# Optimization experiments

Hardware: AMD Instinct MI355X
Metric: run time of the kernel (lower is better)

Reference implementation:

```python
import jax, jax.numpy as jnp
import numpy as np

N, C, H = 256, 128, 4
D = C // H


def setup_inputs() -> dict:
    key = jax.random.key(0)
    ks = jax.random.split(key, 7)
    pair_rep = jax.random.normal(ks[0], (N, N, C), dtype=jnp.float32)
    distance_matrix = jax.random.normal(ks[1], (N, N), dtype=jnp.float32)
    Wqkv = jax.random.normal(ks[2], (C, 3 * C), dtype=jnp.float32) * (1.0 / np.sqrt(C))
    bqkv = jax.random.normal(ks[3], (3 * C,), dtype=jnp.float32) * 0.02
    Wout = jax.random.normal(ks[4], (C, C), dtype=jnp.float32) * (1.0 / np.sqrt(C))
    bout = jax.random.normal(ks[5], (C,), dtype=jnp.float32) * 0.02
    dscale = jnp.ones((1,), dtype=jnp.float32)
    mask = jax.random.randint(ks[6], (N, N), 0, 2).astype(jnp.bool_)
    return {"pair_rep": pair_rep, "distance_matrix": distance_matrix, "Wqkv": Wqkv,
            "bqkv": bqkv, "Wout": Wout, "bout": bout, "dscale": dscale, "mask": mask}


def reference(pair_rep, distance_matrix, Wqkv, bqkv, Wout, bout, dscale, mask):
    n = pair_rep.shape[0]
    qkv = pair_rep @ Wqkv + bqkv                      # [n,n,3c]
    q, k, v = jnp.split(qkv, 3, axis=-1)
    q = q.reshape(n, n, H, D)
    k = k.reshape(n, n, H, D)
    v = v.reshape(n, n, H, D)
    # scores[h,i,j,k] = q[i,j,h,:] . k[i,k,h,:] / sqrt(D)
    scores = jnp.einsum('ijhd,ikhd->hijk', q, k) / np.sqrt(D)
    bias = (dscale[0] * distance_matrix)[None, None, :, :]   # [1,1,n,n]
    scores = scores + bias
    scores = jnp.where(mask[None, None, :, :], -jnp.inf, scores)
    attn = jax.nn.softmax(scores, axis=-1)            # [H,n,n,n]
    out = jnp.einsum('hijk,ikhd->ijhd', attn, v).reshape(n, n, C)
    return out @ Wout + bout
```

## Files before the change

### kernel.cpp

```cpp
#include <hip/hip_runtime.h>
#include <hip/hip_bf16.h>
#include <math.h>

#define NN 256
#define CC 128
#define HH 4
#define DD 32

typedef uint4 u128;
typedef __bf16 bf16x8 __attribute__((ext_vector_type(8)));
typedef float f32x4 __attribute__((ext_vector_type(4)));

#define LOG2E 1.4426950408889634f
#define QSC (0.17677669529663687f * LOG2E)

__global__ __launch_bounds__(256) void prep_kernel(
    const float* __restrict__ dm, const int* __restrict__ mask,
    const float* __restrict__ dscale,
    const float* __restrict__ Wqkv, const float* __restrict__ Wout,
    float* __restrict__ bias2,
    __hip_bfloat16* __restrict__ Wt_qkv, __hip_bfloat16* __restrict__ Wt_out)
{
    const int b = blockIdx.x, t = threadIdx.x;
    if (b < 256) {
        const int j = b, k = t;
        int idx = j * 256 + k;
        float v = mask[idx] ? -INFINITY : dscale[0] * dm[idx] * LOG2E;
        int c = k >> 5, bb = (k >> 4) & 1, quad = (k >> 2) & 3, r = k & 3;
        int dst = ((((c * 2 + bb) * 16 + (j >> 4)) * 64) + quad * 16 + (j & 15)) * 4 + r;
        bias2[dst] = v;
    } else if (b < 448) {
        int idx = (b - 256) * 256 + t;
        int n = idx >> 7, k = idx & 127;
        Wt_qkv[idx] = __float2bfloat16(Wqkv[(size_t)k * 384 + n]);
    } else {
        int idx = (b - 448) * 256 + t;
        int n = idx >> 7, k = idx & 127;
        Wt_out[idx] = __float2bfloat16(Wout[(size_t)k * CC + n]);
    }
}

__global__ __launch_bounds__(512, 2) void qkv_mfma_kernel(
    const float* __restrict__ A,
    const __hip_bfloat16* __restrict__ Bt,
    const float* __restrict__ bias,
    __hip_bfloat16* __restrict__ out)
{
    __shared__ __align__(16) __hip_bfloat16 As[128][136];
    __shared__ __align__(16) __hip_bfloat16 Bs[96][136];
    const int t = threadIdx.x;
    const int m0 = blockIdx.x * 128;

    float4 va[8];
    #pragma unroll
    for (int it = 0; it < 8; ++it) {
        int idx = it * 512 + t;
        int r = idx >> 5, c4 = (idx & 31) * 4;
        va[it] = *(const float4*)(A + (size_t)(m0 + r) * CC + c4);
    }
    #pragma unroll
    for (int it = 0; it < 8; ++it) {
        int idx = it * 512 + t;
        int r = idx >> 5, c4 = (idx & 31) * 4;
        __hip_bfloat162 a01 = __float22bfloat162_rn(float2{va[it].x, va[it].y});
        __hip_bfloat162 a23 = __float22bfloat162_rn(float2{va[it].z, va[it].w});
        uint2 pk;
        pk.x = *(unsigned int*)&a01;
        pk.y = *(unsigned int*)&a23;
        *(uint2*)&As[r][c4] = pk;
    }
    #pragma unroll
    for (int it = 0; it < 3; ++it) {
        int idx = it * 512 + t;
        int n = idx >> 4, c8 = (idx & 15) * 8;
        *(u128*)&Bs[n][c8] = *(const u128*)(Bt + (size_t)n * CC + c8);
    }
    __syncthreads();

    const int w = t >> 6, lane = t & 63;
    const int n16 = lane & 15, quad = lane >> 4;
    const int mw = (w & 3) * 32, nw = (w >> 2) * 48;

    bf16x8 pf[2][4];
    #pragma unroll
    for (int mt = 0; mt < 2; ++mt)
        #pragma unroll
        for (int ks = 0; ks < 4; ++ks)
            pf[mt][ks] = *(const bf16x8*)&As[mw + mt * 16 + n16][ks * 32 + quad * 8];

    for (int nc = 0; nc < 4; ++nc) {
        const int n0 = nc * 96;

        f32x4 acc[2][3];
        #pragma unroll
        for (int mt = 0; mt < 2; ++mt)
            #pragma unroll
            for (int nt = 0; nt < 3; ++nt) acc[mt][nt] = (f32x4){0.f, 0.f, 0.f, 0.f};

        #pragma unroll
        for (int nt = 0; nt < 3; ++nt) {
            bf16x8 wf[4];
            #pragma unroll
            for (int ks = 0; ks < 4; ++ks)
                wf[ks] = *(const bf16x8*)&Bs[nw + nt * 16 + n16][ks * 32 + quad * 8];
            #pragma unroll
            for (int ks = 0; ks < 4; ++ks)
                #pragma unroll
                for (int mt = 0; mt < 2; ++mt)
                    acc[mt][nt] = __builtin_amdgcn_mfma_f32_16x16x32_bf16(wf[ks], pf[mt][ks], acc[mt][nt], 0, 0, 0);
        }
        __syncthreads();

        u128 breg[3];
        if (nc < 3) {
            #pragma unroll
            for (int it = 0; it < 3; ++it) {
                int idx = it * 512 + t;
                int n = idx >> 4, c8 = (idx & 15) * 8;
                breg[it] = *(const u128*)(Bt + (size_t)(n0 + 96 + n) * CC + c8);
            }
        }

        #pragma unroll
        for (int nt = 0; nt < 3; ++nt) {
            int nbase = n0 + nw + nt * 16 + quad * 4;
            float4 b4 = *(const float4*)(bias + nbase);
            float sc = (nbase < CC) ? QSC : 1.0f;
            #pragma unroll
            for (int mt = 0; mt < 2; ++mt) {
                int m = m0 + mw + mt * 16 + n16;
                __hip_bfloat162 h01 = __float22bfloat162_rn(float2{(acc[mt][nt][0] + b4.x) * sc, (acc[mt][nt][1] + b4.y) * sc});
                __hip_bfloat162 h23 = __float22bfloat162_rn(float2{(acc[mt][nt][2] + b4.z) * sc, (acc[mt][nt][3] + b4.w) * sc});
                uint2 pk;
                pk.x = *(unsigned int*)&h01;
                pk.y = *(unsigned int*)&h23;
                *(uint2*)&out[(size_t)m * 384 + nbase] = pk;
            }
        }

        if (nc < 3) {
            #pragma unroll
            for (int it = 0; it < 3; ++it) {
                int idx = it * 512 + t;
                int n = idx >> 4, c8 = (idx & 15) * 8;
                *(u128*)&Bs[n][c8] = breg[it];
            }
            __syncthreads();
        }
    }
}

__global__ __launch_bounds__(512, 8) void attn_mfma_kernel(
    const __hip_bfloat16* __restrict__ qkv,
    const float* __restrict__ bias2,
    __hip_bfloat16* __restrict__ attn_out)
{
    __shared__ __align__(16) __hip_bfloat16 Ks[NN][40];
    __shared__ __align__(16) __hip_bfloat16 VTs[DD][264];

    const int bi = blockIdx.x;
    const int i = bi >> 2, h = bi & 3;
    const int t = threadIdx.x;

    {
        const int r = t >> 1, half = t & 1;
        const __hip_bfloat16* base = qkv + (size_t)(i * NN + r) * 384 + h * DD;
        const u128* ksrc = (const u128*)(base + CC) + half * 2;
        u128* kdst = (u128*)&Ks[r][0] + half * 2;
        kdst[0] = ksrc[0];
        kdst[1] = ksrc[1];
        const u128* vsrc = (const u128*)(base + 2 * CC) + half * 2;
        u128 vr[2];
        vr[0] = vsrc[0];
        vr[1] = vsrc[1];
        const __hip_bfloat16* vh = (const __hip_bfloat16*)vr;
        const int pr = (r & ~0x1F) | ((r & 0xC) << 1) | ((r & 0x10) >> 2) | (r & 0x3);
        #pragma unroll
        for (int dd = 0; dd < 16; ++dd) VTs[half * 16 + dd][pr] = vh[dd];
    }
    __syncthreads();

    const int w = t >> 6, lane = t & 63;
    const int n16 = lane & 15, quad = lane >> 4;

    #pragma unroll
    for (int jt = 0; jt < 2; ++jt) {
        const int j0 = w * 32 + jt * 16;
        const int j = j0 + n16;
        const int jblk = w * 2 + jt;

        bf16x8 qa = *(const bf16x8*)(qkv + (size_t)(i * NN + j) * 384 + h * DD + quad * 8);
        const float4* bb = (const float4*)bias2;

        f32x4 sm = {0.f, 0.f, 0.f, 0.f};
        f32x4 o0 = {0.f, 0.f, 0.f, 0.f}, o1 = {0.f, 0.f, 0.f, 0.f};

        #pragma unroll 2
        for (int c = 0; c < 8; ++c) {
            float4 b0 = bb[((c * 2 + 0) * 16 + jblk) * 64 + lane];
            float4 b1 = bb[((c * 2 + 1) * 16 + jblk) * 64 + lane];
            bf16x8 kb0 = *(const bf16x8*)&Ks[c * 32 + n16][quad * 8];
            bf16x8 kb1 = *(const bf16x8*)&Ks[c * 32 + 16 + n16][quad * 8];
            f32x4 s0 = __builtin_amdgcn_mfma_f32_16x16x32_bf16(
                kb0, qa, (f32x4){b0.x, b0.y, b0.z, b0.w}, 0, 0, 0);
            f32x4 s1 = __builtin_amdgcn_mfma_f32_16x16x32_bf16(
                kb1, qa, (f32x4){b1.x, b1.y, b1.z, b1.w}, 0, 0, 0);

            float p0 = __builtin_amdgcn_exp2f(s0[0]);
            float p1 = __builtin_amdgcn_exp2f(s0[1]);
            float p2 = __builtin_amdgcn_exp2f(s0[2]);
            float p3 = __builtin_amdgcn_exp2f(s0[3]);
            float p4 = __builtin_amdgcn_exp2f(s1[0]);
            float p5 = __builtin_amdgcn_exp2f(s1[1]);
            float p6 = __builtin_amdgcn_exp2f(s1[2]);
            float p7 = __builtin_amdgcn_exp2f(s1[3]);
            sm[0] += p0 + p4;
            sm[1] += p1 + p5;
            sm[2] += p2 + p6;
            sm[3] += p3 + p7;

            __hip_bfloat162 q01 = __float22bfloat162_rn(float2{p0, p1});
            __hip_bfloat162 q23 = __float22bfloat162_rn(float2{p2, p3});
            __hip_bfloat162 q45 = __float22bfloat162_rn(float2{p4, p5});
            __hip_bfloat162 q67 = __float22bfloat162_rn(float2{p6, p7});
            u128 pk;
            pk.x = *(unsigned int*)&q01;
            pk.y = *(unsigned int*)&q23;
            pk.z = *(unsigned int*)&q45;
            pk.w = *(unsigned int*)&q67;
            bf16x8 pa = *(bf16x8*)&pk;

            bf16x8 vb0 = *(const bf16x8*)&VTs[n16][c * 32 + quad * 8];
            bf16x8 vb1 = *(const bf16x8*)&VTs[16 + n16][c * 32 + quad * 8];
            o0 = __builtin_amdgcn_mfma_f32_16x16x32_bf16(vb0, pa, o0, 0, 0, 0);
            o1 = __builtin_amdgcn_mfma_f32_16x16x32_bf16(vb1, pa, o1, 0, 0, 0);
        }

        float sum = (sm[0] + sm[1]) + (sm[2] + sm[3]);
        sum += __shfl_xor(sum, 16);
        sum += __shfl_xor(sum, 32);
        float inv = 1.0f / sum;

        __hip_bfloat16* obase = attn_out + (size_t)(i * NN + j) * CC + h * DD + quad * 4;
        {
            __hip_bfloat162 h01 = __float22bfloat162_rn(float2{o0[0] * inv, o0[1] * inv});
            __hip_bfloat162 h23 = __float22bfloat162_rn(float2{o0[2] * inv, o0[3] * inv});
            uint2 pk;
            pk.x = *(unsigned int*)&h01;
            pk.y = *(unsigned int*)&h23;
            *(uint2*)(obase) = pk;
        }
        {
            __hip_bfloat162 h01 = __float22bfloat162_rn(float2{o1[0] * inv, o1[1] * inv});
            __hip_bfloat162 h23 = __float22bfloat162_rn(float2{o1[2] * inv, o1[3] * inv});
            uint2 pk;
            pk.x = *(unsigned int*)&h01;
            pk.y = *(unsigned int*)&h23;
            *(uint2*)(obase + 16) = pk;
        }
    }
}

__global__ __launch_bounds__(512, 4) void out_mfma_kernel(
    const __hip_bfloat16* __restrict__ A,
    const __hip_bfloat16* __restrict__ Bt,
    const float* __restrict__ bias,
    float* __restrict__ out)
{
    __shared__ __align__(16) __hip_bfloat16 As[128][136];
    __shared__ __align__(16) __hip_bfloat16 Bs[128][136];
    const int t = threadIdx.x;
    const int m0 = blockIdx.x * 128;

    u128 ra[4], rb[4];
    #pragma unroll
    for (int it = 0; it < 4; ++it) {
        int idx = it * 512 + t;
        int r = idx >> 4, c8 = (idx & 15) * 8;
        ra[it] = *(const u128*)(A + (size_t)(m0 + r) * CC + c8);
    }
    #pragma unroll
    for (int it = 0; it < 4; ++it) {
        int idx = it * 512 + t;
        int n = idx >> 4, c8 = (idx & 15) * 8;
        rb[it] = *(const u128*)(Bt + (size_t)n * CC + c8);
    }
    #pragma unroll
    for (int it = 0; it < 4; ++it) {
        int idx = it * 512 + t;
        int r = idx >> 4, c8 = (idx & 15) * 8;
        *(u128*)&As[r][c8] = ra[it];
    }
    #pragma unroll
    for (int it = 0; it < 4; ++it) {
        int idx = it * 512 + t;
        int n = idx >> 4, c8 = (idx & 15) * 8;
        *(u128*)&Bs[n][c8] = rb[it];
    }
    __syncthreads();

    const int w = t >> 6, lane = t & 63;
    const int n16 = lane & 15, quad = lane >> 4;
    const int mw = (w & 3) * 32, nw = (w >> 2) * 64;

    bf16x8 pf[2][4];
    #pragma unroll
    for (int mt = 0; mt < 2; ++mt)
        #pragma unroll
        for (int ks = 0; ks < 4; ++ks)
            pf[mt][ks] = *(const bf16x8*)&As[mw + mt * 16 + n16][ks * 32 + quad * 8];

    f32x4 acc[2][4];
    #pragma unroll
    for (int mt = 0; mt < 2; ++mt)
        #pragma unroll
        for (int nt = 0; nt < 4; ++nt) acc[mt][nt] = (f32x4){0.f, 0.f, 0.f, 0.f};

    #pragma unroll
    for (int nt = 0; nt < 4; ++nt) {
        bf16x8 wf[4];
        #pragma unroll
        for (int ks = 0; ks < 4; ++ks)
            wf[ks] = *(const bf16x8*)&Bs[nw + nt * 16 + n16][ks * 32 + quad * 8];
        #pragma unroll
        for (int ks = 0; ks < 4; ++ks)
            #pragma unroll
            for (int mt = 0; mt < 2; ++mt)
                acc[mt][nt] = __builtin_amdgcn_mfma_f32_16x16x32_bf16(wf[ks], pf[mt][ks], acc[mt][nt], 0, 0, 0);
    }

    #pragma unroll
    for (int nt = 0; nt < 4; ++nt) {
        int nbase = nw + nt * 16 + quad * 4;
        float4 b4 = *(const float4*)(bias + nbase);
        #pragma unroll
        for (int mt = 0; mt < 2; ++mt) {
            int m = m0 + mw + mt * 16 + n16;
            float4 ov;
            ov.x = acc[mt][nt][0] + b4.x;
            ov.y = acc[mt][nt][1] + b4.y;
            ov.z = acc[mt][nt][2] + b4.z;
            ov.w = acc[mt][nt][3] + b4.w;
            *(float4*)&out[(size_t)m * CC + nbase] = ov;
        }
    }
}

extern "C" void kernel_launch(void* const* d_in, const int* in_sizes, int n_in,
                              void* d_out, int out_size, void* d_ws, size_t ws_size,
                              hipStream_t stream) {
    const float* pair_rep = (const float*)d_in[0];
    const float* dm       = (const float*)d_in[1];
    const float* Wqkv     = (const float*)d_in[2];
    const float* bqkv     = (const float*)d_in[3];
    const float* Wout     = (const float*)d_in[4];
    const float* bout     = (const float*)d_in[5];
    const float* dscale   = (const float*)d_in[6];
    const int*   mask     = (const int*)d_in[7];
    float* out = (float*)d_out;

    char* p = (char*)d_ws;
    float* bias2 = (float*)p;                 p += (size_t)NN * NN * 4;
    __hip_bfloat16* Wt_qkv = (__hip_bfloat16*)p;  p += (size_t)384 * CC * 2;
    __hip_bfloat16* Wt_out = (__hip_bfloat16*)p;  p += (size_t)CC * CC * 2;
    __hip_bfloat16* qkv  = (__hip_bfloat16*)p;    p += (size_t)65536 * 384 * 2;
    __hip_bfloat16* attn = (__hip_bfloat16*)p;

    prep_kernel<<<dim3(512), dim3(256), 0, stream>>>(dm, mask, dscale, Wqkv, Wout, bias2, Wt_qkv, Wt_out);
    qkv_mfma_kernel<<<dim3(512), dim3(512), 0, stream>>>(pair_rep, Wt_qkv, bqkv, qkv);
    attn_mfma_kernel<<<dim3(1024), dim3(512), 0, stream>>>(qkv, bias2, attn);
    out_mfma_kernel<<<dim3(512), dim3(512), 0, stream>>>(attn, Wt_out, bout, out);
}
```

Measured before the change: 146.4 us.

## Process two query rows per attention block to reuse bias loads

Each attention block now handles two i rows for one head, staging both K and V^T tiles in shared memory and sharing each bias2 load across the two rows' score MFMAs. The grid halves to 512 blocks, and the launch bounds drop to 4 blocks per CU to allow more registers. The aim is to halve global bias traffic per unit of work and add instruction-level parallelism. In exchange it doubles LDS per block and raises register pressure, and the smaller grid may leave compute units underfilled.

```diff
diff --git a/kernel.cpp b/kernel.cpp
--- a/kernel.cpp
+++ b/kernel.cpp
@@ -150,38 +150,38 @@
     }
 }
 
-__global__ __launch_bounds__(512, 8) void attn_mfma_kernel(
+__global__ __launch_bounds__(512, 4) void attn_mfma_kernel(
     const __hip_bfloat16* __restrict__ qkv,
     const float* __restrict__ bias2,
     __hip_bfloat16* __restrict__ attn_out)
 {
-    __shared__ __align__(16) __hip_bfloat16 Ks[NN][40];
-    __shared__ __align__(16) __hip_bfloat16 VTs[DD][264];
+    __shared__ __align__(16) __hip_bfloat16 Ks[2][NN][40];
+    __shared__ __align__(16) __hip_bfloat16 VTs[2][DD][264];
 
     const int bi = blockIdx.x;
-    const int i = bi >> 2, h = bi & 3;
+    const int h = bi >> 7, ip = bi & 127;
+    const int i0 = ip * 2;
     const int t = threadIdx.x;
-
-    {
-        const int r = t >> 1, half = t & 1;
-        const __hip_bfloat16* base = qkv + (size_t)(i * NN + r) * 384 + h * DD;
-        const u128* ksrc = (const u128*)(base + CC) + half * 2;
-        u128* kdst = (u128*)&Ks[r][0] + half * 2;
-        kdst[0] = ksrc[0];
-        kdst[1] = ksrc[1];
-        const u128* vsrc = (const u128*)(base + 2 * CC) + half * 2;
-        u128 vr[2];
-        vr[0] = vsrc[0];
-        vr[1] = vsrc[1];
-        const __hip_bfloat16* vh = (const __hip_bfloat16*)vr;
-        const int pr = (r & ~0x1F) | ((r & 0xC) << 1) | ((r & 0x10) >> 2) | (r & 0x3);
-        #pragma unroll
-        for (int dd = 0; dd < 16; ++dd) VTs[half * 16 + dd][pr] = vh[dd];
-    }
-    __syncthreads();
-
     const int w = t >> 6, lane = t & 63;
     const int n16 = lane & 15, quad = lane >> 4;
+
+    #pragma unroll
+    for (int ii = 0; ii < 2; ++ii) {
+        const int i = i0 + ii;
+        #pragma unroll
+        for (int it = 0; it < 2; ++it) {
+            int idx = it * 512 + t;
+            int row = idx >> 2, q4 = idx & 3;
+            const __hip_bfloat16* base = qkv + ((size_t)i * NN + row) * 384 + h * DD;
+            *(u128*)&Ks[ii][row][q4 * 8] = *(const u128*)(base + CC + q4 * 8);
+            u128 vr = *(const u128*)(base + 2 * CC + q4 * 8);
+            const __hip_bfloat16* vh = (const __hip_bfloat16*)&vr;
+            int pr = (row & ~0x1F) | ((row & 0xC) << 1) | ((row & 0x10) >> 2) | (row & 0x3);
+            #pragma unroll
+            for (int dd = 0; dd < 8; ++dd) VTs[ii][q4 * 8 + dd][pr] = vh[dd];
+        }
+    }
+    __syncthreads();
 
     #pragma unroll
     for (int jt = 0; jt < 2; ++jt) {
@@ -189,74 +189,123 @@
         const int j = j0 + n16;
         const int jblk = w * 2 + jt;
 
-        bf16x8 qa = *(const bf16x8*)(qkv + (size_t)(i * NN + j) * 384 + h * DD + quad * 8);
+        bf16x8 qa0 = *(const bf16x8*)(qkv + ((size_t)i0 * NN + j) * 384 + h * DD + quad * 8);
+        bf16x8 qa1 = *(const bf16x8*)(qkv + ((size_t)(i0 + 1) * NN + j) * 384 + h * DD + quad * 8);
         const float4* bb = (const float4*)bias2;
 
-        f32x4 sm = {0.f, 0.f, 0.f, 0.f};
-        f32x4 o0 = {0.f, 0.f, 0.f, 0.f}, o1 = {0.f, 0.f, 0.f, 0.f};
+        f32x4 sm0 = {0.f, 0.f, 0.f, 0.f}, sm1 = {0.f, 0.f, 0.f, 0.f};
+        f32x4 o00 = {0.f, 0.f, 0.f, 0.f}, o01 = {0.f, 0.f, 0.f, 0.f};
+        f32x4 o10 = {0.f, 0.f, 0.f, 0.f}, o11 = {0.f, 0.f, 0.f, 0.f};
 
         #pragma unroll 2
         for (int c = 0; c < 8; ++c) {
             float4 b0 = bb[((c * 2 + 0) * 16 + jblk) * 64 + lane];
             float4 b1 = bb[((c * 2 + 1) * 16 + jblk) * 64 + lane];
-            bf16x8 kb0 = *(const bf16x8*)&Ks[c * 32 + n16][quad * 8];
-            bf16x8 kb1 = *(const bf16x8*)&Ks[c * 32 + 16 + n16][quad * 8];
-            f32x4 s0 = __builtin_amdgcn_mfma_f32_16x16x32_bf16(
-                kb0, qa, (f32x4){b0.x, b0.y, b0.z, b0.w}, 0, 0, 0);
-            f32x4 s1 = __builtin_amdgcn_mfma_f32_16x16x32_bf16(
-                kb1, qa, (f32x4){b1.x, b1.y, b1.z, b1.w}, 0, 0, 0);
-
-            float p0 = __builtin_amdgcn_exp2f(s0[0]);
-            float p1 = __builtin_amdgcn_exp2f(s0[1]);
-            float p2 = __builtin_amdgcn_exp2f(s0[2]);
-            float p3 = __builtin_amdgcn_exp2f(s0[3]);
-            float p4 = __builtin_amdgcn_exp2f(s1[0]);
-            float p5 = __builtin_amdgcn_exp2f(s1[1]);
-            float p6 = __builtin_amdgcn_exp2f(s1[2]);
-            float p7 = __builtin_amdgcn_exp2f(s1[3]);
-            sm[0] += p0 + p4;
-            sm[1] += p1 + p5;
-            sm[2] += p2 + p6;
-            sm[3] += p3 + p7;
-
-            __hip_bfloat162 q01 = __float22bfloat162_rn(float2{p0, p1});
-            __hip_bfloat162 q23 = __float22bfloat162_rn(float2{p2, p3});
-            __hip_bfloat162 q45 = __float22bfloat162_rn(float2{p4, p5});
-            __hip_bfloat162 q67 = __float22bfloat162_rn(float2{p6, p7});
-            u128 pk;
-            pk.x = *(unsigned int*)&q01;
-            pk.y = *(unsigned int*)&q23;
-            pk.z = *(unsigned int*)&q45;
-            pk.w = *(unsigned int*)&q67;
-            bf16x8 pa = *(bf16x8*)&pk;
-
-            bf16x8 vb0 = *(const bf16x8*)&VTs[n16][c * 32 + quad * 8];
-            bf16x8 vb1 = *(const bf16x8*)&VTs[16 + n16][c * 32 + quad * 8];
-            o0 = __builtin_amdgcn_mfma_f32_16x16x32_bf16(vb0, pa, o0, 0, 0, 0);
-            o1 = __builtin_amdgcn_mfma_f32_16x16x32_bf16(vb1, pa, o1, 0, 0, 0);
-        }
-
-        float sum = (sm[0] + sm[1]) + (sm[2] + sm[3]);
-        sum += __shfl_xor(sum, 16);
-        sum += __shfl_xor(sum, 32);
-        float inv = 1.0f / sum;
-
-        __hip_bfloat16* obase = attn_out + (size_t)(i * NN + j) * CC + h * DD + quad * 4;
+            bf16x8 kb00 = *(const bf16x8*)&Ks[0][c * 32 + n16][quad * 8];
+            bf16x8 kb01 = *(const bf16x8*)&Ks[0][c * 32 + 16 + n16][quad * 8];
+            bf16x8 kb10 = *(const bf16x8*)&Ks[1][c * 32 + n16][quad * 8];
+            bf16x8 kb11 = *(const bf16x8*)&Ks[1][c * 32 + 16 + n16][quad * 8];
+            f32x4 s00 = __builtin_amdgcn_mfma_f32_16x16x32_bf16(
+                kb00, qa0, (f32x4){b0.x, b0.y, b0.z, b0.w}, 0, 0, 0);
+            f32x4 s01 = __builtin_amdgcn_mfma_f32_16x16x32_bf16(
+                kb01, qa0, (f32x4){b1.x, b1.y, b1.z, b1.w}, 0, 0, 0);
+            f32x4 s10 = __builtin_amdgcn_mfma_f32_16x16x32_bf16(
+                kb10, qa1, (f32x4){b0.x, b0.y, b0.z, b0.w}, 0, 0, 0);
+            f32x4 s11 = __builtin_amdgcn_mfma_f32_16x16x32_bf16(
+                kb11, qa1, (f32x4){b1.x, b1.y, b1.z, b1.w}, 0, 0, 0);
+
+            {
+                float p0 = __builtin_amdgcn_exp2f(s00[0]);
+                float p1 = __builtin_amdgcn_exp2f(s00[1]);
+                float p2 = __builtin_amdgcn_exp2f(s00[2]);
+                float p3 = __builtin_amdgcn_exp2f(s00[3]);
+                float p4 = __builtin_amdgcn_exp2f(s01[0]);
+                float p5 = __builtin_amdgcn_exp2f(s01[1]);
+                float p6 = __builtin_amdgcn_exp2f(s01[2]);
+                float p7 = __builtin_amdgcn_exp2f(s01[3]);
+                sm0[0] += p0 + p4;
+                sm0[1] += p1 + p5;
+                sm0[2] += p2 + p6;
+                sm0[3] += p3 + p7;
+                __hip_bfloat162 q01 = __float22bfloat162_rn(float2{p0, p1});
+                __hip_bfloat162 q23 = __float22bfloat162_rn(float2{p2, p3});
+                __hip_bfloat162 q45 = __float22bfloat162_rn(float2{p4, p5});
+                __hip_bfloat162 q67 = __float22bfloat162_rn(float2{p6, p7});
+                u128 pk;
+                pk.x = *(unsigned int*)&q01;
+                pk.y = *(unsigned int*)&q23;
+                pk.z = *(unsigned int*)&q45;
+                pk.w = *(unsigned int*)&q67;
+                bf16x8 pa = *(bf16x8*)&pk;
+                bf16x8 vb0 = *(const bf16x8*)&VTs[0][n16][c * 32 + quad * 8];
+                bf16x8 vb1 = *(const bf16x8*)&VTs[0][16 + n16][c * 32 + quad * 8];
+                o00 = __builtin_amdgcn_mfma_f32_16x16x32_bf16(vb0, pa, o00, 0, 0, 0);
+                o01 = __builtin_amdgcn_mfma_f32_16x16x32_bf16(vb1, pa, o01, 0, 0, 0);
+            }
+            {
+                float p0 = __builtin_amdgcn_exp2f(s10[0]);
+                float p1 = __builtin_amdgcn_exp2f(s10[1]);
+                float p2 = __builtin_amdgcn_exp2f(s10[2]);
+                float p3 = __builtin_amdgcn_exp2f(s10[3]);
+                float p4 = __builtin_amdgcn_exp2f(s11[0]);
+                float p5 = __builtin_amdgcn_exp2f(s11[1]);
+                float p6 = __builtin_amdgcn_exp2f(s11[2]);
+                float p7 = __builtin_amdgcn_exp2f(s11[3]);
+                sm1[0] += p0 + p4;
+                sm1[1] += p1 + p5;
+                sm1[2] += p2 + p6;
+                sm1[3] += p3 + p7;
+                __hip_bfloat162 q01 = __float22bfloat162_rn(float2{p0, p1});
+                __hip_bfloat162 q23 = __float22bfloat162_rn(float2{p2, p3});
+                __hip_bfloat162 q45 = __float22bfloat162_rn(float2{p4, p5});
+                __hip_bfloat162 q67 = __float22bfloat162_rn(float2{p6, p7});
+                u128 pk;
+                pk.x = *(unsigned int*)&q01;
+                pk.y = *(unsigned int*)&q23;
+                pk.z = *(unsigned int*)&q45;
+                pk.w = *(unsigned int*)&q67;
+                bf16x8 pa = *(bf16x8*)&pk;
+                bf16x8 vb0 = *(const bf16x8*)&VTs[1][n16][c * 32 + quad * 8];
+                bf16x8 vb1 = *(const bf16x8*)&VTs[1][16 + n16][c * 32 + quad * 8];
+                o10 = __builtin_amdgcn_mfma_f32_16x16x32_bf16(vb0, pa, o10, 0, 0, 0);
+                o11 = __builtin_amdgcn_mfma_f32_16x16x32_bf16(vb1, pa, o11, 0, 0, 0);
+            }
+        }
+
+        float sum0 = (sm0[0] + sm0[1]) + (sm0[2] + sm0[3]);
+        sum0 += __shfl_xor(sum0, 16);
+        sum0 += __shfl_xor(sum0, 32);
+        float inv0 = 1.0f / sum0;
+        float sum1 = (sm1[0] + sm1[1]) + (sm1[2] + sm1[3]);
+        sum1 += __shfl_xor(sum1, 16);
+        sum1 += __shfl_xor(sum1, 32);
+        float inv1 = 1.0f / sum1;
+
+        __hip_bfloat16* ob0 = attn_out + ((size_t)i0 * NN + j) * CC + h * DD + quad * 4;
+        __hip_bfloat16* ob1 = attn_out + ((size_t)(i0 + 1) * NN + j) * CC + h * DD + quad * 4;
         {
-            __hip_bfloat162 h01 = __float22bfloat162_rn(float2{o0[0] * inv, o0[1] * inv});
-            __hip_bfloat162 h23 = __float22bfloat162_rn(float2{o0[2] * inv, o0[3] * inv});
-            uint2 pk;
-            pk.x = *(unsigned int*)&h01;
-            pk.y = *(unsigned int*)&h23;
-            *(uint2*)(obase) = pk;
+            __hip_bfloat162 h01 = __float22bfloat162_rn(float2{o00[0] * inv0, o00[1] * inv0});
+            __hip_bfloat162 h23 = __float22bfloat162_rn(float2{o00[2] * inv0, o00[3] * inv0});
+            uint2 pk; pk.x = *(unsigned int*)&h01; pk.y = *(unsigned int*)&h23;
+            *(uint2*)(ob0) = pk;
         }
         {
-            __hip_bfloat162 h01 = __float22bfloat162_rn(float2{o1[0] * inv, o1[1] * inv});
-            __hip_bfloat162 h23 = __float22bfloat162_rn(float2{o1[2] * inv, o1[3] * inv});
-            uint2 pk;
-            pk.x = *(unsigned int*)&h01;
-            pk.y = *(unsigned int*)&h23;
-            *(uint2*)(obase + 16) = pk;
+            __hip_bfloat162 h01 = __float22bfloat162_rn(float2{o01[0] * inv0, o01[1] * inv0});
+            __hip_bfloat162 h23 = __float22bfloat162_rn(float2{o01[2] * inv0, o01[3] * inv0});
+            uint2 pk; pk.x = *(unsigned int*)&h01; pk.y = *(unsigned int*)&h23;
+            *(uint2*)(ob0 + 16) = pk;
+        }
+        {
+            __hip_bfloat162 h01 = __float22bfloat162_rn(float2{o10[0] * inv1, o10[1] * inv1});
+            __hip_bfloat162 h23 = __float22bfloat162_rn(float2{o10[2] * inv1, o10[3] * inv1});
+            uint2 pk; pk.x = *(unsigned int*)&h01; pk.y = *(unsigned int*)&h23;
+            *(uint2*)(ob1) = pk;
+        }
+        {
+            __hip_bfloat162 h01 = __float22bfloat162_rn(float2{o11[0] * inv1, o11[1] * inv1});
+            __hip_bfloat162 h23 = __float22bfloat162_rn(float2{o11[2] * inv1, o11[3] * inv1});
+            uint2 pk; pk.x = *(unsigned int*)&h01; pk.y = *(unsigned int*)&h23;
+            *(uint2*)(ob1 + 16) = pk;
         }
     }
 }
@@ -368,6 +417,6 @@
 
     prep_kernel<<<dim3(512), dim3(256), 0, stream>>>(dm, mask, dscale, Wqkv, Wout, bias2, Wt_qkv, Wt_out);
     qkv_mfma_kernel<<<dim3(512), dim3(512), 0, stream>>>(pair_rep, Wt_qkv, bqkv, qkv);
-    attn_mfma_kernel<<<dim3(1024), dim3(512), 0, stream>>>(qkv, bias2, attn);
+    attn_mfma_kernel<<<dim3(512), dim3(512), 0, stream>>>(qkv, bias2, attn);
     out_mfma_kernel<<<dim3(512), dim3(512), 0, stream>>>(attn, Wt_out, bout, out);
 }
```

Result: faster. 143.4 us (-2.1%).
